# Performance work log

Measured on AMD Instinct MI355X. Metric: run time of the kernel, lower is better.

The kernel has to match this reference:

```python
import jax, jax.numpy as jnp
import numpy as np

B, S, D, H = 4, 2048, 1024, 16
HD = D // H  # 64


def setup_inputs() -> dict:
    key = jax.random.key(0)
    ks = jax.random.split(key, 16)
    inv = 1.0 / np.sqrt(D)
    inv_hd = 1.0 / np.sqrt(D)
    inp = {
        "query": jax.random.normal(ks[0], (B, S, D), jnp.float32),
        "key": jax.random.normal(ks[1], (B, S, D), jnp.float32),
        "value": jax.random.normal(ks[2], (B, S, D), jnp.float32),
        # causal mask: True entries are masked out (masked_fill semantics)
        "mask": jnp.triu(jnp.ones((S, S), jnp.bool_), k=1),
        # weights stored [in, out] (math identical to torch x @ W.T)
        "Wq": jax.random.normal(ks[3], (D, D), jnp.float32) * inv,
        "Wk": jax.random.normal(ks[4], (D, D), jnp.float32) * inv,
        "Wv": jax.random.normal(ks[5], (D, D), jnp.float32) * inv,
        "wq_h": jax.random.normal(ks[6], (D, HD), jnp.float32) * inv_hd,
        "bq_h": jax.random.normal(ks[7], (HD,), jnp.float32) * inv_hd,
        "wk_h": jax.random.normal(ks[8], (D, HD), jnp.float32) * inv_hd,
        "bk_h": jax.random.normal(ks[9], (HD,), jnp.float32) * inv_hd,
        "wv_h": jax.random.normal(ks[10], (D, HD), jnp.float32) * inv_hd,
        "bv_h": jax.random.normal(ks[11], (HD,), jnp.float32) * inv_hd,
        "Wo": jax.random.normal(ks[12], (D, D), jnp.float32) * inv,
    }
    return inp


def reference(query, key, value, mask, Wq, Wk, Wv, wq_h, bq_h, wk_h, bk_h, wv_h, bv_h, Wo):
    # full-width projections
    q = jnp.einsum('bsd,de->bse', query, Wq)
    k = jnp.einsum('bsd,de->bse', key, Wk)
    v = jnp.einsum('bsd,de->bse', value, Wv)
    # per-head projections: the torch loop reuses the SAME weights every
    # iteration, so all H head outputs are identical -> compute once.
    qh = jnp.einsum('bsd,dh->bsh', q, wq_h) + bq_h  # [B,S,HD]
    kh = jnp.einsum('bsd,dh->bsh', k, wk_h) + bk_h
    vh = jnp.einsum('bsd,dh->bsh', v, wv_h) + bv_h
    scores = jnp.einsum('bsh,bth->bst', qh, kh) / jnp.sqrt(jnp.float32(HD))
    scores = jnp.where(mask, jnp.float32(-1e9), scores)
    attn = jax.nn.softmax(scores, axis=-1)
    out_h = jnp.einsum('bst,bth->bsh', attn, vh)  # [B,S,HD]
    out = jnp.tile(out_h, (1, 1, H))  # cat of H identical heads -> [B,S,D]
    # final linear; dropout is identity at inference
    return jnp.einsum('bsd,de->bse', out, Wo)
```

## Files before the change

### kernel.cpp

```cpp
#include <hip/hip_runtime.h>
#include <math.h>

#define S_LEN 2048
#define BATCH 4
#define DMODEL 1024
#define HDIM 64
#define NROWS (BATCH * S_LEN)

typedef __attribute__((ext_vector_type(8))) short bf16x8;
typedef __attribute__((ext_vector_type(4))) float f32x4;

__device__ inline ushort f2bf(float f) {
    union { float f; uint u; } v{f};
    uint r = v.u + 0x7fffu + ((v.u >> 16) & 1u);
    return (ushort)(r >> 16);
}

__device__ inline bf16x8 cvt8(float4 a, float4 b) {
    bf16x8 r;
    r[0] = (short)f2bf(a.x); r[1] = (short)f2bf(a.y);
    r[2] = (short)f2bf(a.z); r[3] = (short)f2bf(a.w);
    r[4] = (short)f2bf(b.x); r[5] = (short)f2bf(b.y);
    r[6] = (short)f2bf(b.z); r[7] = (short)f2bf(b.w);
    return r;
}

__global__ __launch_bounds__(256) void transpose_wh(
    const float* __restrict__ B0, const float* __restrict__ B1, const float* __restrict__ B2,
    ushort* __restrict__ T0, ushort* __restrict__ T1, ushort* __restrict__ T2)
{
    const int z = blockIdx.y;
    const float* B = (z == 0) ? B0 : (z == 1) ? B1 : B2;
    ushort* T      = (z == 0) ? T0 : (z == 1) ? T1 : T2;
    const int kr0 = blockIdx.x * 64;
    __shared__ ushort Ts[64][72];
    const int t = threadIdx.x;

    #pragma unroll
    for (int q = 0; q < 4; ++q) {
        int u   = t * 4 + q;
        int row = u >> 4;
        int c4  = (u & 15) << 2;
        float4 v = *reinterpret_cast<const float4*>(
            B + (size_t)(kr0 + row) * 64 + c4);
        Ts[row][c4 + 0] = f2bf(v.x); Ts[row][c4 + 1] = f2bf(v.y);
        Ts[row][c4 + 2] = f2bf(v.z); Ts[row][c4 + 3] = f2bf(v.w);
    }
    __syncthreads();
    #pragma unroll
    for (int q = 0; q < 2; ++q) {
        int u  = t * 2 + q;
        int h  = u >> 3;
        int k8 = (u & 7) << 3;
        uint4 o;
        uint* ow = reinterpret_cast<uint*>(&o);
        #pragma unroll
        for (int i = 0; i < 4; ++i)
            ow[i] = (uint)Ts[k8 + 2 * i][h] | ((uint)Ts[k8 + 2 * i + 1][h] << 16);
        *reinterpret_cast<uint4*>(T + (size_t)h * 1024 + kr0 + k8) = o;
    }
}

__global__ __launch_bounds__(256) void prep_direct(
    const float* __restrict__ A0, const float* __restrict__ A1, const float* __restrict__ A2,
    const ushort* __restrict__ W0, const ushort* __restrict__ W1, const ushort* __restrict__ W2,
    ushort* __restrict__ T0, ushort* __restrict__ T1, ushort* __restrict__ T2)
{
    const int z = blockIdx.y;
    const float* A  = (z == 0) ? A0 : (z == 1) ? A1 : A2;
    const ushort* W = (z == 0) ? W0 : (z == 1) ? W1 : W2;
    ushort* T       = (z == 0) ? T0 : (z == 1) ? T1 : T2;

    __shared__ float Pr[4][16][64];

    const int t    = threadIdx.x;
    const int w    = t >> 6;
    const int lane = t & 63;
    const int lg   = lane >> 4;
    const int lc   = lane & 15;
    const int r0   = blockIdx.x * 16;

    const float*  Ap = A + (size_t)(r0 + lc) * 1024 + (w << 8) + (lg << 3);
    const ushort* Bp = W + (size_t)lc * 1024 + (w << 8) + (lg << 3);

    f32x4 acc[4] = {};
    float4 a0[2], a1[2];
    uint4  bl[2][4];

    #pragma unroll
    for (int d = 0; d < 2; ++d) {
        a0[d] = *reinterpret_cast<const float4*>(Ap + d * 32);
        a1[d] = *reinterpret_cast<const float4*>(Ap + d * 32 + 4);
        #pragma unroll
        for (int n = 0; n < 4; ++n)
            bl[d][n] = *reinterpret_cast<const uint4*>(Bp + n * 16384 + d * 32);
    }

    #pragma unroll
    for (int ks = 0; ks < 8; ++ks) {
        const int d = ks & 1;
        bf16x8 af = cvt8(a0[d], a1[d]);
        bf16x8 bfr[4];
        #pragma unroll
        for (int n = 0; n < 4; ++n)
            bfr[n] = __builtin_bit_cast(bf16x8, bl[d][n]);
        if (ks < 6) {
            a0[d] = *reinterpret_cast<const float4*>(Ap + (ks + 2) * 32);
            a1[d] = *reinterpret_cast<const float4*>(Ap + (ks + 2) * 32 + 4);
            #pragma unroll
            for (int n = 0; n < 4; ++n)
                bl[d][n] = *reinterpret_cast<const uint4*>(Bp + n * 16384 + (ks + 2) * 32);
        }
        #pragma unroll
        for (int n = 0; n < 4; ++n)
            acc[n] = __builtin_amdgcn_mfma_f32_16x16x32_bf16(af, bfr[n], acc[n], 0, 0, 0);
    }

    #pragma unroll
    for (int n = 0; n < 4; ++n)
        #pragma unroll
        for (int reg = 0; reg < 4; ++reg)
            Pr[w][4 * lg + reg][16 * n + lc] = acc[n][reg];
    __syncthreads();

    const int row = t >> 4;
    const int col = (t & 15) << 2;
    float s[4];
    #pragma unroll
    for (int i = 0; i < 4; ++i)
        s[i] = Pr[0][row][col + i] + Pr[1][row][col + i] +
               Pr[2][row][col + i] + Pr[3][row][col + i];
    #pragma unroll
    for (int i = 0; i < 4; ++i)
        T[(size_t)(col + i) * 1024 + r0 + row] = f2bf(s[i]);
}

__global__ __launch_bounds__(256) void proj_direct(
    const float* __restrict__ A0, const float* __restrict__ A1, const float* __restrict__ A2,
    const ushort* __restrict__ W0, const ushort* __restrict__ W1, const ushort* __restrict__ W2,
    const float* __restrict__ b0, const float* __restrict__ b1, const float* __restrict__ b2,
    ushort* __restrict__ O0, ushort* __restrict__ O1, ushort* __restrict__ O2)
{
    const int z = blockIdx.y;
    const float* A    = (z == 0) ? A0 : (z == 1) ? A1 : A2;
    const ushort* W   = (z == 0) ? W0 : (z == 1) ? W1 : W2;
    const float* bias = (z == 0) ? b0 : (z == 1) ? b1 : b2;
    ushort* O         = (z == 0) ? O0 : (z == 1) ? O1 : O2;

    __shared__ float Pr[4][16][64];

    const int t    = threadIdx.x;
    const int w    = t >> 6;
    const int lane = t & 63;
    const int lg   = lane >> 4;
    const int lc   = lane & 15;
    const int r0   = blockIdx.x * 16;

    const float*  Ap = A + (size_t)(r0 + lc) * 1024 + (w << 8) + (lg << 3);
    const ushort* Bp = W + (size_t)lc * 1024 + (w << 8) + (lg << 3);

    f32x4 acc[4] = {};
    float4 a0[2], a1[2];
    uint4  bl[2][4];

    #pragma unroll
    for (int d = 0; d < 2; ++d) {
        a0[d] = *reinterpret_cast<const float4*>(Ap + d * 32);
        a1[d] = *reinterpret_cast<const float4*>(Ap + d * 32 + 4);
        #pragma unroll
        for (int n = 0; n < 4; ++n)
            bl[d][n] = *reinterpret_cast<const uint4*>(Bp + n * 16384 + d * 32);
    }

    #pragma unroll
    for (int ks = 0; ks < 8; ++ks) {
        const int d = ks & 1;
        bf16x8 af = cvt8(a0[d], a1[d]);
        bf16x8 bfr[4];
        #pragma unroll
        for (int n = 0; n < 4; ++n)
            bfr[n] = __builtin_bit_cast(bf16x8, bl[d][n]);
        if (ks < 6) {
            a0[d] = *reinterpret_cast<const float4*>(Ap + (ks + 2) * 32);
            a1[d] = *reinterpret_cast<const float4*>(Ap + (ks + 2) * 32 + 4);
            #pragma unroll
            for (int n = 0; n < 4; ++n)
                bl[d][n] = *reinterpret_cast<const uint4*>(Bp + n * 16384 + (ks + 2) * 32);
        }
        #pragma unroll
        for (int n = 0; n < 4; ++n)
            acc[n] = __builtin_amdgcn_mfma_f32_16x16x32_bf16(af, bfr[n], acc[n], 0, 0, 0);
    }

    #pragma unroll
    for (int n = 0; n < 4; ++n)
        #pragma unroll
        for (int reg = 0; reg < 4; ++reg)
            Pr[w][4 * lg + reg][16 * n + lc] = acc[n][reg];
    __syncthreads();

    const int row = t >> 4;
    const int col = (t & 15) << 2;
    float4 bb = *reinterpret_cast<const float4*>(bias + col);
    float s0 = Pr[0][row][col + 0] + Pr[1][row][col + 0] + Pr[2][row][col + 0] + Pr[3][row][col + 0] + bb.x;
    float s1 = Pr[0][row][col + 1] + Pr[1][row][col + 1] + Pr[2][row][col + 1] + Pr[3][row][col + 1] + bb.y;
    float s2 = Pr[0][row][col + 2] + Pr[1][row][col + 2] + Pr[2][row][col + 2] + Pr[3][row][col + 2] + bb.z;
    float s3 = Pr[0][row][col + 3] + Pr[1][row][col + 3] + Pr[2][row][col + 3] + Pr[3][row][col + 3] + bb.w;
    ushort4 o;
    o.x = f2bf(s0); o.y = f2bf(s1); o.z = f2bf(s2); o.w = f2bf(s3);
    *reinterpret_cast<ushort4*>(O + (size_t)(r0 + row) * 64 + col) = o;
}

__global__ __launch_bounds__(256) void fold_wo(const float* __restrict__ Wo,
                                               ushort* __restrict__ WoT)
{
    int idx = blockIdx.x * 256 + threadIdx.x;
    int j = idx >> 10;
    int e = idx & 1023;
    float s = 0.f;
    #pragma unroll
    for (int h = 0; h < 16; ++h)
        s += Wo[(size_t)((h << 6) + j) * 1024 + e];
    WoT[(size_t)e * 64 + j] = f2bf(s);
}

__global__ __launch_bounds__(256) void transpose_v(const ushort* __restrict__ vh,
                                                   ushort* __restrict__ vhT)
{
    const int b  = blockIdx.y;
    const int r0 = blockIdx.x * 64;
    __shared__ ushort T[64][72];
    const int t = threadIdx.x;

    #pragma unroll
    for (int q = 0; q < 2; ++q) {
        int u  = t * 2 + q;
        int s  = u >> 3;
        int d8 = (u & 7) << 3;
        uint4 v = *reinterpret_cast<const uint4*>(
            vh + ((size_t)b * S_LEN + r0 + s) * 64 + d8);
        *reinterpret_cast<uint4*>(&T[s][d8]) = v;
    }
    __syncthreads();
    #pragma unroll
    for (int q = 0; q < 2; ++q) {
        int u  = t * 2 + q;
        int d  = u >> 3;
        int s8 = (u & 7) << 3;
        uint4 o;
        uint* ow = reinterpret_cast<uint*>(&o);
        #pragma unroll
        for (int i = 0; i < 4; ++i)
            ow[i] = (uint)T[s8 + 2 * i][d] | ((uint)T[s8 + 2 * i + 1][d] << 16);
        *reinterpret_cast<uint4*>(
            vhT + (size_t)b * 64 * S_LEN + (size_t)d * S_LEN + r0 + s8) = o;
    }
}

__global__ __launch_bounds__(256) void flash_mfma(
    const ushort* __restrict__ qh, const ushort* __restrict__ kh,
    const ushort* __restrict__ vhT,
    float* __restrict__ Opart, float* __restrict__ mpart, float* __restrict__ lpart)
{
    const int b = blockIdx.y;
    const int u = blockIdx.x;
    int gi = 0;
    #pragma unroll
    for (int gg = 0; gg < 7; ++gg)
        if (u >= 2 * (gg + 1) * (gg + 2)) gi = gg + 1;
    const int rem = u - 2 * gi * (gi + 1);
    const int dq  = rem / (gi + 1);
    const int c   = rem - dq * (gi + 1);
    const int qt  = 4 * gi + dq;
    const int r0  = qt * 64;
    const int kvbase = c << 8;
    const int slot = b * 144 + u;

    __shared__ ushort Qs[64][72];
    __shared__ ushort Ks[64][72];
    __shared__ ushort Vt[64][72];
    __shared__ ushort Pw[4][16][72];

    const int t    = threadIdx.x;
    const int w    = t >> 6;
    const int lane = t & 63;
    const int lg   = lane >> 4;
    const int lc   = lane & 15;

    const ushort* qb  = qh  + (size_t)b * S_LEN * 64;
    const ushort* kb  = kh  + (size_t)b * S_LEN * 64;
    const ushort* vtb = vhT + (size_t)b * 64 * S_LEN;

    #pragma unroll
    for (int q = 0; q < 2; ++q) {
        int uu  = t * 2 + q;
        int row = uu >> 3;
        int c8  = (uu & 7) << 3;
        *reinterpret_cast<uint4*>(&Qs[row][c8]) =
            *reinterpret_cast<const uint4*>(qb + (size_t)(r0 + row) * 64 + c8);
    }
    __syncthreads();
    bf16x8 qf0 = *reinterpret_cast<const bf16x8*>(&Qs[16 * w + lc][lg * 8]);
    bf16x8 qf1 = *reinterpret_cast<const bf16x8*>(&Qs[16 * w + lc][32 + lg * 8]);

    f32x4 od[4] = {};
    float m = -INFINITY, lsum = 0.f;
    const int qrow = r0 + 16 * w + lc;

    const int ntt = min(4, ((r0 + 63 - kvbase) >> 6) + 1);
    for (int tt = 0; tt < ntt; ++tt) {
        const int t0 = kvbase + (tt << 6);
        __syncthreads();
        #pragma unroll
        for (int q = 0; q < 2; ++q) {
            int uu  = t * 2 + q;
            int row = uu >> 3;
            int c8  = (uu & 7) << 3;
            *reinterpret_cast<uint4*>(&Ks[row][c8]) =
                *reinterpret_cast<const uint4*>(kb + (size_t)(t0 + row) * 64 + c8);
            *reinterpret_cast<uint4*>(&Vt[row][c8]) =
                *reinterpret_cast<const uint4*>(vtb + (size_t)row * S_LEN + t0 + c8);
        }
        __syncthreads();

        if (t0 <= r0 + 16 * w + 15) {
            f32x4 s[4] = {};
            #pragma unroll
            for (int a = 0; a < 4; ++a) {
                bf16x8 kf0 = *reinterpret_cast<const bf16x8*>(&Ks[16 * a + lc][lg * 8]);
                bf16x8 kf1 = *reinterpret_cast<const bf16x8*>(&Ks[16 * a + lc][32 + lg * 8]);
                s[a] = __builtin_amdgcn_mfma_f32_16x16x32_bf16(kf0, qf0, s[a], 0, 0, 0);
                s[a] = __builtin_amdgcn_mfma_f32_16x16x32_bf16(kf1, qf1, s[a], 0, 0, 0);
            }
            float rm = -1e30f;
            #pragma unroll
            for (int a = 0; a < 4; ++a)
                #pragma unroll
                for (int reg = 0; reg < 4; ++reg) {
                    int kv = t0 + 16 * a + 4 * lg + reg;
                    float v = s[a][reg] * 0.125f;
                    if (kv > qrow) v = -1e30f;
                    s[a][reg] = v;
                    rm = fmaxf(rm, v);
                }
            rm = fmaxf(rm, __shfl_xor(rm, 16));
            rm = fmaxf(rm, __shfl_xor(rm, 32));
            float mn = fmaxf(m, rm);
            float sc = __expf(m - mn);
            float rs = 0.f;
            #pragma unroll
            for (int a = 0; a < 4; ++a)
                #pragma unroll
                for (int reg = 0; reg < 4; ++reg) {
                    float p = __expf(s[a][reg] - mn);
                    s[a][reg] = p;
                    rs += p;
                }
            rs += __shfl_xor(rs, 16);
            rs += __shfl_xor(rs, 32);
            lsum = lsum * sc + rs;
            m = mn;
            #pragma unroll
            for (int di = 0; di < 4; ++di) od[di] *= sc;

            #pragma unroll
            for (int a = 0; a < 4; ++a)
                #pragma unroll
                for (int rp = 0; rp < 2; ++rp) {
                    uint pk = (uint)f2bf(s[a][2 * rp]) |
                              ((uint)f2bf(s[a][2 * rp + 1]) << 16);
                    *reinterpret_cast<uint*>(&Pw[w][lc][16 * a + 4 * lg + 2 * rp]) = pk;
                }
            bf16x8 pf0 = *reinterpret_cast<const bf16x8*>(&Pw[w][lc][lg * 8]);
            bf16x8 pf1 = *reinterpret_cast<const bf16x8*>(&Pw[w][lc][32 + lg * 8]);
            #pragma unroll
            for (int di = 0; di < 4; ++di) {
                bf16x8 vf0 = *reinterpret_cast<const bf16x8*>(&Vt[16 * di + lc][lg * 8]);
                bf16x8 vf1 = *reinterpret_cast<const bf16x8*>(&Vt[16 * di + lc][32 + lg * 8]);
                od[di] = __builtin_amdgcn_mfma_f32_16x16x32_bf16(vf0, pf0, od[di], 0, 0, 0);
                od[di] = __builtin_amdgcn_mfma_f32_16x16x32_bf16(vf1, pf1, od[di], 0, 0, 0);
            }
        }
    }

    #pragma unroll
    for (int di = 0; di < 4; ++di)
        #pragma unroll
        for (int reg = 0; reg < 4; ++reg)
            Opart[(size_t)slot * 4096 + (16 * di + 4 * lg + reg) * 64 + 16 * w + lc] =
                od[di][reg];
    if (lg == 0) {
        mpart[slot * 64 + 16 * w + lc] = m;
        lpart[slot * 64 + 16 * w + lc] = lsum;
    }
}

__global__ __launch_bounds__(256) void flash_combine(
    const float* __restrict__ Opart, const float* __restrict__ mpart,
    const float* __restrict__ lpart, ushort* __restrict__ oh)
{
    const int qt = blockIdx.x, b = blockIdx.y;
    const int gi = qt >> 2;
    const int nc = gi + 1;
    const int ubase = 2 * gi * (gi + 1) + (qt & 3) * (gi + 1);
    __shared__ float T[64][65];

    const int t  = threadIdx.x;
    const int q  = t & 63;
    const int d0 = (t >> 6) << 4;

    float mc[8];
    float M = -INFINITY;
    #pragma unroll
    for (int cc = 0; cc < 8; ++cc) {
        mc[cc] = (cc < nc) ? mpart[(b * 144 + ubase + cc) * 64 + q] : -INFINITY;
        M = fmaxf(M, mc[cc]);
    }
    float L = 0.f;
    float acc[16] = {};
    for (int cc = 0; cc < nc; ++cc) {
        const int slot = b * 144 + ubase + cc;
        float wgt = __expf(mc[cc] - M);
        L += lpart[slot * 64 + q] * wgt;
        const float* op = Opart + (size_t)slot * 4096 + q;
        #pragma unroll
        for (int i = 0; i < 16; ++i)
            acc[i] += wgt * op[(d0 + i) * 64];
    }
    float inv = 1.f / L;
    #pragma unroll
    for (int i = 0; i < 16; ++i) T[q][d0 + i] = acc[i] * inv;
    __syncthreads();

    const int q2 = t >> 2;
    const int ds = (t & 3) << 4;
    uint wbuf[8];
    #pragma unroll
    for (int i = 0; i < 8; ++i)
        wbuf[i] = (uint)f2bf(T[q2][ds + 2 * i]) |
                  ((uint)f2bf(T[q2][ds + 2 * i + 1]) << 16);
    ushort* dst = oh + ((size_t)b * S_LEN + qt * 64 + q2) * 64 + ds;
    uint4 o1, o2;
    o1.x = wbuf[0]; o1.y = wbuf[1]; o1.z = wbuf[2]; o1.w = wbuf[3];
    o2.x = wbuf[4]; o2.y = wbuf[5]; o2.z = wbuf[6]; o2.w = wbuf[7];
    *reinterpret_cast<uint4*>(dst)     = o1;
    *reinterpret_cast<uint4*>(dst + 8) = o2;
}

__global__ __launch_bounds__(256) void epilogue_mfma(
    const ushort* __restrict__ oh, const ushort* __restrict__ WoT,
    float* __restrict__ out)
{
    const int r0 = blockIdx.x * 64;
    const int c0 = blockIdx.y * 128;
    __shared__ ushort As[64][72];
    __shared__ ushort Bs[128][72];

    const int t    = threadIdx.x;
    const int w    = t >> 6;
    const int lane = t & 63;
    const int lg   = lane >> 4;
    const int lc   = lane & 15;

    #pragma unroll
    for (int q = 0; q < 2; ++q) {
        int u   = t * 2 + q;
        int row = u >> 3;
        int c8  = (u & 7) << 3;
        *reinterpret_cast<uint4*>(&As[row][c8]) =
            *reinterpret_cast<const uint4*>(oh + (size_t)(r0 + row) * 64 + c8);
    }
    #pragma unroll
    for (int q = 0; q < 4; ++q) {
        int u   = t * 4 + q;
        int row = u >> 3;
        int c8  = (u & 7) << 3;
        *reinterpret_cast<uint4*>(&Bs[row][c8]) =
            *reinterpret_cast<const uint4*>(WoT + (size_t)(c0 + row) * 64 + c8);
    }
    __syncthreads();

    bf16x8 af0 = *reinterpret_cast<const bf16x8*>(&As[16 * w + lc][lg * 8]);
    bf16x8 af1 = *reinterpret_cast<const bf16x8*>(&As[16 * w + lc][32 + lg * 8]);
    f32x4 acc[8] = {};
    #pragma unroll
    for (int n = 0; n < 8; ++n) {
        bf16x8 bf0 = *reinterpret_cast<const bf16x8*>(&Bs[16 * n + lc][lg * 8]);
        bf16x8 bf1 = *reinterpret_cast<const bf16x8*>(&Bs[16 * n + lc][32 + lg * 8]);
        acc[n] = __builtin_amdgcn_mfma_f32_16x16x32_bf16(af0, bf0, acc[n], 0, 0, 0);
        acc[n] = __builtin_amdgcn_mfma_f32_16x16x32_bf16(af1, bf1, acc[n], 0, 0, 0);
    }
    #pragma unroll
    for (int n = 0; n < 8; ++n)
        #pragma unroll
        for (int reg = 0; reg < 4; ++reg)
            out[(size_t)(r0 + 16 * w + 4 * lg + reg) * 1024 + c0 + 16 * n + lc] =
                acc[n][reg];
}

extern "C" void kernel_launch(void* const* d_in, const int* in_sizes, int n_in,
                              void* d_out, int out_size, void* d_ws, size_t ws_size,
                              hipStream_t stream)
{
    const float* query = (const float*)d_in[0];
    const float* key   = (const float*)d_in[1];
    const float* value = (const float*)d_in[2];
    const float* Wq   = (const float*)d_in[4];
    const float* Wk   = (const float*)d_in[5];
    const float* Wv   = (const float*)d_in[6];
    const float* wq_h = (const float*)d_in[7];
    const float* bq_h = (const float*)d_in[8];
    const float* wk_h = (const float*)d_in[9];
    const float* bk_h = (const float*)d_in[10];
    const float* wv_h = (const float*)d_in[11];
    const float* bv_h = (const float*)d_in[12];
    const float* Wo   = (const float*)d_in[13];
    float* out = (float*)d_out;

    ushort* W16  = (ushort*)d_ws;
    ushort* WT0  = W16;
    ushort* WT1  = W16 + 65536;
    ushort* WT2  = W16 + 131072;
    ushort* WoT  = W16 + 196608;
    ushort* qh   = W16 + 262144;
    ushort* kh   = qh + 524288;
    ushort* vh   = kh + 524288;
    ushort* vhT  = vh + 524288;
    ushort* oh   = vhT + 524288;
    ushort* whT0 = oh + 524288;
    ushort* whT1 = whT0 + 65536;
    ushort* whT2 = whT1 + 65536;

    float* Opart = out;
    float* mpart = out + 2359296;
    float* lpart = out + 2396160;

    transpose_wh<<<dim3(16, 3), 256, 0, stream>>>(
        wq_h, wk_h, wv_h, whT0, whT1, whT2);
    fold_wo<<<256, 256, 0, stream>>>(Wo, WoT);

    prep_direct<<<dim3(64, 3), 256, 0, stream>>>(
        Wq, Wk, Wv, whT0, whT1, whT2, WT0, WT1, WT2);

    proj_direct<<<dim3(512, 3), 256, 0, stream>>>(
        query, key, value, WT0, WT1, WT2, bq_h, bk_h, bv_h, qh, kh, vh);

    transpose_v<<<dim3(S_LEN / 64, BATCH), 256, 0, stream>>>(vh, vhT);

    flash_mfma<<<dim3(144, BATCH), 256, 0, stream>>>(
        qh, kh, vhT, Opart, mpart, lpart);
    flash_combine<<<dim3(S_LEN / 64, BATCH), 256, 0, stream>>>(
        Opart, mpart, lpart, oh);

    epilogue_mfma<<<dim3(NROWS / 64, DMODEL / 128), 256, 0, stream>>>(oh, WoT, out);
}
```

Baseline: 83.56 us.

## Stream projection activations through LDS with async global_load_lds and swizzle

The per-row projection kernel now loads its whole slice of folded weights into registers up front, then issues all activation loads as asynchronous global-to-LDS copies with an XOR swizzle. Each 64-column chunk is consumed once its copies land, using staged vmcnt waits, so MFMA work overlaps the remaining loads. The aim is deeper memory-level parallelism on the activation stream, which dominates this memory-bound kernel. In exchange it adds 64KB of LDS per block and a large register footprint for the weight fragments, both of which cut occupancy.

```diff
diff --git a/kernel.cpp b/kernel.cpp
--- a/kernel.cpp
+++ b/kernel.cpp
@@ -9,6 +9,9 @@
 
 typedef __attribute__((ext_vector_type(8))) short bf16x8;
 typedef __attribute__((ext_vector_type(4))) float f32x4;
+
+#define GLP(p) ((const __attribute__((address_space(1))) unsigned int*)(p))
+#define LDP(p) ((__attribute__((address_space(3))) unsigned int*)(p))
 
 __device__ inline ushort f2bf(float f) {
     union { float f; uint u; } v{f};
@@ -135,7 +138,7 @@
         T[(size_t)(col + i) * 1024 + r0 + row] = f2bf(s[i]);
 }
 
-__global__ __launch_bounds__(256) void proj_direct(
+__global__ __launch_bounds__(256) void proj_stream(
     const float* __restrict__ A0, const float* __restrict__ A1, const float* __restrict__ A2,
     const ushort* __restrict__ W0, const ushort* __restrict__ W1, const ushort* __restrict__ W2,
     const float* __restrict__ b0, const float* __restrict__ b1, const float* __restrict__ b2,
@@ -147,6 +150,7 @@
     const float* bias = (z == 0) ? b0 : (z == 1) ? b1 : b2;
     ushort* O         = (z == 0) ? O0 : (z == 1) ? O1 : O2;
 
+    __shared__ __align__(16) char StageRaw[65536];
     __shared__ float Pr[4][16][64];
 
     const int t    = threadIdx.x;
@@ -154,43 +158,66 @@
     const int lane = t & 63;
     const int lg   = lane >> 4;
     const int lc   = lane & 15;
+    const int rx   = lc & 7;
     const int r0   = blockIdx.x * 16;
 
-    const float*  Ap = A + (size_t)(r0 + lc) * 1024 + (w << 8) + (lg << 3);
-    const ushort* Bp = W + (size_t)lc * 1024 + (w << 8) + (lg << 3);
+    bf16x8 bB[4][4][2];
+    #pragma unroll
+    for (int c = 0; c < 4; ++c)
+        #pragma unroll
+        for (int n = 0; n < 4; ++n)
+            #pragma unroll
+            for (int h = 0; h < 2; ++h)
+                bB[c][n][h] = *reinterpret_cast<const bf16x8*>(
+                    W + (size_t)(16 * n + lc) * 1024 + (w << 8) + (c << 6) +
+                    h * 32 + lg * 8);
+    asm volatile("s_waitcnt vmcnt(0)" ::: "memory");
+    __builtin_amdgcn_sched_barrier(0);
+
+    #pragma unroll
+    for (int c = 0; c < 4; ++c)
+        #pragma unroll
+        for (int p = 0; p < 4; ++p) {
+            int u   = p * 64 + lane;
+            int row = u >> 4;
+            int pos = u & 15;
+            int g   = (pos & 8) | ((pos & 7) ^ (row & 7));
+            __builtin_amdgcn_global_load_lds(
+                GLP(A + (size_t)(r0 + row) * 1024 + (w << 8) + (c << 6) + g * 4),
+                LDP(StageRaw + (size_t)w * 16384 + c * 4096 + p * 1024),
+                16, 0, 0);
+        }
 
     f32x4 acc[4] = {};
-    float4 a0[2], a1[2];
-    uint4  bl[2][4];
-
-    #pragma unroll
-    for (int d = 0; d < 2; ++d) {
-        a0[d] = *reinterpret_cast<const float4*>(Ap + d * 32);
-        a1[d] = *reinterpret_cast<const float4*>(Ap + d * 32 + 4);
-        #pragma unroll
-        for (int n = 0; n < 4; ++n)
-            bl[d][n] = *reinterpret_cast<const uint4*>(Bp + n * 16384 + d * 32);
-    }
-
-    #pragma unroll
-    for (int ks = 0; ks < 8; ++ks) {
-        const int d = ks & 1;
-        bf16x8 af = cvt8(a0[d], a1[d]);
-        bf16x8 bfr[4];
-        #pragma unroll
-        for (int n = 0; n < 4; ++n)
-            bfr[n] = __builtin_bit_cast(bf16x8, bl[d][n]);
-        if (ks < 6) {
-            a0[d] = *reinterpret_cast<const float4*>(Ap + (ks + 2) * 32);
-            a1[d] = *reinterpret_cast<const float4*>(Ap + (ks + 2) * 32 + 4);
-            #pragma unroll
-            for (int n = 0; n < 4; ++n)
-                bl[d][n] = *reinterpret_cast<const uint4*>(Bp + n * 16384 + (ks + 2) * 32);
-        }
-        #pragma unroll
-        for (int n = 0; n < 4; ++n)
-            acc[n] = __builtin_amdgcn_mfma_f32_16x16x32_bf16(af, bfr[n], acc[n], 0, 0, 0);
-    }
+    const float4* lpw = reinterpret_cast<const float4*>(
+        StageRaw + (size_t)w * 16384);
+
+#define PROJ_CHUNK(c, VM)                                                     \
+    {                                                                         \
+        asm volatile("s_waitcnt vmcnt(" #VM ")" ::: "memory");                \
+        __builtin_amdgcn_sched_barrier(0);                                    \
+        const float4* lp = lpw + (c) * 256 + lc * 16;                         \
+        float4 f0 = lp[( (lg * 2 + 0) ^ rx)];                                 \
+        float4 f1 = lp[( (lg * 2 + 1) ^ rx)];                                 \
+        float4 f2 = lp[(8 | ((lg * 2 + 0) ^ rx))];                            \
+        float4 f3 = lp[(8 | ((lg * 2 + 1) ^ rx))];                            \
+        bf16x8 a0 = cvt8(f0, f1);                                             \
+        bf16x8 a1 = cvt8(f2, f3);                                             \
+        acc[0] = __builtin_amdgcn_mfma_f32_16x16x32_bf16(a0, bB[c][0][0], acc[0], 0, 0, 0); \
+        acc[0] = __builtin_amdgcn_mfma_f32_16x16x32_bf16(a1, bB[c][0][1], acc[0], 0, 0, 0); \
+        acc[1] = __builtin_amdgcn_mfma_f32_16x16x32_bf16(a0, bB[c][1][0], acc[1], 0, 0, 0); \
+        acc[1] = __builtin_amdgcn_mfma_f32_16x16x32_bf16(a1, bB[c][1][1], acc[1], 0, 0, 0); \
+        acc[2] = __builtin_amdgcn_mfma_f32_16x16x32_bf16(a0, bB[c][2][0], acc[2], 0, 0, 0); \
+        acc[2] = __builtin_amdgcn_mfma_f32_16x16x32_bf16(a1, bB[c][2][1], acc[2], 0, 0, 0); \
+        acc[3] = __builtin_amdgcn_mfma_f32_16x16x32_bf16(a0, bB[c][3][0], acc[3], 0, 0, 0); \
+        acc[3] = __builtin_amdgcn_mfma_f32_16x16x32_bf16(a1, bB[c][3][1], acc[3], 0, 0, 0); \
+    }
+
+    PROJ_CHUNK(0, 12)
+    PROJ_CHUNK(1, 8)
+    PROJ_CHUNK(2, 4)
+    PROJ_CHUNK(3, 0)
+#undef PROJ_CHUNK
 
     #pragma unroll
     for (int n = 0; n < 4; ++n)
@@ -542,7 +569,7 @@
     prep_direct<<<dim3(64, 3), 256, 0, stream>>>(
         Wq, Wk, Wv, whT0, whT1, whT2, WT0, WT1, WT2);
 
-    proj_direct<<<dim3(512, 3), 256, 0, stream>>>(
+    proj_stream<<<dim3(512, 3), 256, 0, stream>>>(
         query, key, value, WT0, WT1, WT2, bq_h, bk_h, bv_h, qh, kh, vh);
 
     transpose_v<<<dim3(S_LEN / 64, BATCH), 256, 0, stream>>>(vh, vhT);
```

Measured after the change: 83.16 us. No clear change (-0.5%).

## Rewrite projection kernel as single-wave blocks with swizzled LDS A staging

Applied to the files above, without the earlier changes.

The fused-weight projection kernel moves from four waves splitting K (with an LDS cross-wave reduction) to one 64-thread wave per 16-row block that walks the full K=1024. A tiles are loaded with coalesced float4 row reads, converted to bf16, and staged through a double-buffered XOR-swizzled LDS buffer to reach the MFMA operand layout, which removes the shared-memory partial-sum reduction and the block barrier. The tradeoff is fewer threads per block and a longer serial K loop per wave. Weight fragments are now read directly per chunk without prefetch, and no barrier protects the LDS reuse, which is only safe because the block is a single wave.

```diff
diff --git a/kernel.cpp b/kernel.cpp
--- a/kernel.cpp
+++ b/kernel.cpp
@@ -135,7 +135,7 @@
         T[(size_t)(col + i) * 1024 + r0 + row] = f2bf(s[i]);
 }
 
-__global__ __launch_bounds__(256) void proj_direct(
+__global__ __launch_bounds__(64) void proj_sw(
     const float* __restrict__ A0, const float* __restrict__ A1, const float* __restrict__ A2,
     const ushort* __restrict__ W0, const ushort* __restrict__ W1, const ushort* __restrict__ W2,
     const float* __restrict__ b0, const float* __restrict__ b1, const float* __restrict__ b2,
@@ -147,68 +147,75 @@
     const float* bias = (z == 0) ? b0 : (z == 1) ? b1 : b2;
     ushort* O         = (z == 0) ? O0 : (z == 1) ? O1 : O2;
 
-    __shared__ float Pr[4][16][64];
-
-    const int t    = threadIdx.x;
-    const int w    = t >> 6;
-    const int lane = t & 63;
-    const int lg   = lane >> 4;
-    const int lc   = lane & 15;
-    const int r0   = blockIdx.x * 16;
-
-    const float*  Ap = A + (size_t)(r0 + lc) * 1024 + (w << 8) + (lg << 3);
-    const ushort* Bp = W + (size_t)lc * 1024 + (w << 8) + (lg << 3);
+    __shared__ __align__(16) ushort Abuf[2][16][64];
+
+    const int l  = threadIdx.x;
+    const int lg = l >> 4;
+    const int lc = l & 15;
+    const int wu = lc >> 1;
+    const int wh = lc & 1;
+    const int r0 = blockIdx.x * 16;
 
     f32x4 acc[4] = {};
-    float4 a0[2], a1[2];
-    uint4  bl[2][4];
-
-    #pragma unroll
-    for (int d = 0; d < 2; ++d) {
-        a0[d] = *reinterpret_cast<const float4*>(Ap + d * 32);
-        a1[d] = *reinterpret_cast<const float4*>(Ap + d * 32 + 4);
-        #pragma unroll
-        for (int n = 0; n < 4; ++n)
-            bl[d][n] = *reinterpret_cast<const uint4*>(Bp + n * 16384 + d * 32);
-    }
-
-    #pragma unroll
-    for (int ks = 0; ks < 8; ++ks) {
-        const int d = ks & 1;
-        bf16x8 af = cvt8(a0[d], a1[d]);
-        bf16x8 bfr[4];
-        #pragma unroll
-        for (int n = 0; n < 4; ++n)
-            bfr[n] = __builtin_bit_cast(bf16x8, bl[d][n]);
-        if (ks < 6) {
-            a0[d] = *reinterpret_cast<const float4*>(Ap + (ks + 2) * 32);
-            a1[d] = *reinterpret_cast<const float4*>(Ap + (ks + 2) * 32 + 4);
-            #pragma unroll
-            for (int n = 0; n < 4; ++n)
-                bl[d][n] = *reinterpret_cast<const uint4*>(Bp + n * 16384 + (ks + 2) * 32);
-        }
-        #pragma unroll
-        for (int n = 0; n < 4; ++n)
-            acc[n] = __builtin_amdgcn_mfma_f32_16x16x32_bf16(af, bfr[n], acc[n], 0, 0, 0);
-    }
-
-    #pragma unroll
-    for (int n = 0; n < 4; ++n)
+
+#define LOADA(R, c)                                                           \
+    _Pragma("unroll")                                                         \
+    for (int j = 0; j < 4; ++j)                                               \
+        R[j] = *reinterpret_cast<const float4*>(                              \
+            A + (size_t)(r0 + 4 * j + lg) * 1024 + (c) * 64 + lc * 4);
+
+#define PROCESS(c, R, BUF)                                                    \
+    {                                                                         \
+        bf16x8 bfr[4][2];                                                     \
+        _Pragma("unroll")                                                     \
+        for (int a = 0; a < 4; ++a)                                           \
+            _Pragma("unroll")                                                 \
+            for (int s = 0; s < 2; ++s)                                       \
+                bfr[a][s] = *reinterpret_cast<const bf16x8*>(                 \
+                    W + (size_t)(16 * a + lc) * 1024 + (c) * 64 + s * 32 +    \
+                    lg * 8);                                                  \
+        _Pragma("unroll")                                                     \
+        for (int j = 0; j < 4; ++j) {                                         \
+            uint2 pk;                                                         \
+            pk.x = (uint)f2bf(R[j].x) | ((uint)f2bf(R[j].y) << 16);           \
+            pk.y = (uint)f2bf(R[j].z) | ((uint)f2bf(R[j].w) << 16);           \
+            int row = 4 * j + lg;                                             \
+            char* dst = (char*)Abuf + (BUF) * 2048 + row * 128 +              \
+                        ((wu ^ (row & 7)) << 4) + wh * 8;                     \
+            *reinterpret_cast<uint2*>(dst) = pk;                              \
+        }                                                                     \
+        _Pragma("unroll")                                                     \
+        for (int s = 0; s < 2; ++s) {                                         \
+            const char* src = (const char*)Abuf + (BUF) * 2048 + lc * 128 +   \
+                              (((s * 4 + lg) ^ (lc & 7)) << 4);               \
+            bf16x8 af = *reinterpret_cast<const bf16x8*>(src);                \
+            _Pragma("unroll")                                                 \
+            for (int a = 0; a < 4; ++a)                                       \
+                acc[a] = __builtin_amdgcn_mfma_f32_16x16x32_bf16(             \
+                    af, bfr[a][s], acc[a], 0, 0, 0);                          \
+        }                                                                     \
+    }
+
+    float4 ra[4], rb[4];
+    LOADA(ra, 0)
+    #pragma unroll
+    for (int cc = 0; cc < 8; ++cc) {
+        LOADA(rb, 2 * cc + 1)
+        PROCESS(2 * cc, ra, 0)
+        if (cc < 7) LOADA(ra, 2 * cc + 2)
+        PROCESS(2 * cc + 1, rb, 1)
+    }
+#undef LOADA
+#undef PROCESS
+
+    #pragma unroll
+    for (int a = 0; a < 4; ++a) {
+        float bv = bias[16 * a + lc];
         #pragma unroll
         for (int reg = 0; reg < 4; ++reg)
-            Pr[w][4 * lg + reg][16 * n + lc] = acc[n][reg];
-    __syncthreads();
-
-    const int row = t >> 4;
-    const int col = (t & 15) << 2;
-    float4 bb = *reinterpret_cast<const float4*>(bias + col);
-    float s0 = Pr[0][row][col + 0] + Pr[1][row][col + 0] + Pr[2][row][col + 0] + Pr[3][row][col + 0] + bb.x;
-    float s1 = Pr[0][row][col + 1] + Pr[1][row][col + 1] + Pr[2][row][col + 1] + Pr[3][row][col + 1] + bb.y;
-    float s2 = Pr[0][row][col + 2] + Pr[1][row][col + 2] + Pr[2][row][col + 2] + Pr[3][row][col + 2] + bb.z;
-    float s3 = Pr[0][row][col + 3] + Pr[1][row][col + 3] + Pr[2][row][col + 3] + Pr[3][row][col + 3] + bb.w;
-    ushort4 o;
-    o.x = f2bf(s0); o.y = f2bf(s1); o.z = f2bf(s2); o.w = f2bf(s3);
-    *reinterpret_cast<ushort4*>(O + (size_t)(r0 + row) * 64 + col) = o;
+            O[(size_t)(r0 + 4 * lg + reg) * 64 + 16 * a + lc] =
+                f2bf(acc[a][reg] + bv);
+    }
 }
 
 __global__ __launch_bounds__(256) void fold_wo(const float* __restrict__ Wo,
@@ -542,7 +549,7 @@
     prep_direct<<<dim3(64, 3), 256, 0, stream>>>(
         Wq, Wk, Wv, whT0, whT1, whT2, WT0, WT1, WT2);
 
-    proj_direct<<<dim3(512, 3), 256, 0, stream>>>(
+    proj_sw<<<dim3(512, 3), 64, 0, stream>>>(
         query, key, value, WT0, WT1, WT2, bq_h, bk_h, bv_h, qh, kh, vh);
 
     transpose_v<<<dim3(S_LEN / 64, BATCH), 256, 0, stream>>>(vh, vhT);
```

Result: slower. 85.81 us (+2.7%).

## Replace split-K register projection with LDS-tiled 64-row MFMA GEMM

Applied to the files above, without the earlier changes.

The fused per-head projection kernel no longer splits K across four waves with register prefetch and an LDS reduction. Each block now takes 64 rows, stages bf16-converted A tiles and weight tiles in shared memory per 64-wide K step, and each wave computes its own 16 rows over the full K. This lets the 64x1024 weight tile be shared by 64 rows instead of 16 and removes the cross-wave partial-sum reduction. In exchange it adds two barriers per K step, has no global-load prefetch, and launches a quarter as many blocks.

```diff
diff --git a/kernel.cpp b/kernel.cpp
--- a/kernel.cpp
+++ b/kernel.cpp
@@ -135,80 +135,73 @@
         T[(size_t)(col + i) * 1024 + r0 + row] = f2bf(s[i]);
 }
 
-__global__ __launch_bounds__(256) void proj_direct(
+__global__ __launch_bounds__(256) void proj_mfma(
     const float* __restrict__ A0, const float* __restrict__ A1, const float* __restrict__ A2,
     const ushort* __restrict__ W0, const ushort* __restrict__ W1, const ushort* __restrict__ W2,
     const float* __restrict__ b0, const float* __restrict__ b1, const float* __restrict__ b2,
     ushort* __restrict__ O0, ushort* __restrict__ O1, ushort* __restrict__ O2)
 {
     const int z = blockIdx.y;
-    const float* A    = (z == 0) ? A0 : (z == 1) ? A1 : A2;
-    const ushort* W   = (z == 0) ? W0 : (z == 1) ? W1 : W2;
+    const float* A  = (z == 0) ? A0 : (z == 1) ? A1 : A2;
+    const ushort* W = (z == 0) ? W0 : (z == 1) ? W1 : W2;
     const float* bias = (z == 0) ? b0 : (z == 1) ? b1 : b2;
-    ushort* O         = (z == 0) ? O0 : (z == 1) ? O1 : O2;
-
-    __shared__ float Pr[4][16][64];
+    ushort* O       = (z == 0) ? O0 : (z == 1) ? O1 : O2;
+
+    __shared__ ushort As[64][72];
+    __shared__ ushort Bs[64][72];
 
     const int t    = threadIdx.x;
     const int w    = t >> 6;
     const int lane = t & 63;
     const int lg   = lane >> 4;
     const int lc   = lane & 15;
-    const int r0   = blockIdx.x * 16;
-
-    const float*  Ap = A + (size_t)(r0 + lc) * 1024 + (w << 8) + (lg << 3);
-    const ushort* Bp = W + (size_t)lc * 1024 + (w << 8) + (lg << 3);
+    const int r0   = blockIdx.x * 64;
 
     f32x4 acc[4] = {};
-    float4 a0[2], a1[2];
-    uint4  bl[2][4];
-
-    #pragma unroll
-    for (int d = 0; d < 2; ++d) {
-        a0[d] = *reinterpret_cast<const float4*>(Ap + d * 32);
-        a1[d] = *reinterpret_cast<const float4*>(Ap + d * 32 + 4);
-        #pragma unroll
-        for (int n = 0; n < 4; ++n)
-            bl[d][n] = *reinterpret_cast<const uint4*>(Bp + n * 16384 + d * 32);
-    }
-
-    #pragma unroll
-    for (int ks = 0; ks < 8; ++ks) {
-        const int d = ks & 1;
-        bf16x8 af = cvt8(a0[d], a1[d]);
-        bf16x8 bfr[4];
-        #pragma unroll
-        for (int n = 0; n < 4; ++n)
-            bfr[n] = __builtin_bit_cast(bf16x8, bl[d][n]);
-        if (ks < 6) {
-            a0[d] = *reinterpret_cast<const float4*>(Ap + (ks + 2) * 32);
-            a1[d] = *reinterpret_cast<const float4*>(Ap + (ks + 2) * 32 + 4);
-            #pragma unroll
-            for (int n = 0; n < 4; ++n)
-                bl[d][n] = *reinterpret_cast<const uint4*>(Bp + n * 16384 + (ks + 2) * 32);
-        }
-        #pragma unroll
-        for (int n = 0; n < 4; ++n)
-            acc[n] = __builtin_amdgcn_mfma_f32_16x16x32_bf16(af, bfr[n], acc[n], 0, 0, 0);
-    }
-
-    #pragma unroll
-    for (int n = 0; n < 4; ++n)
-        #pragma unroll
-        for (int reg = 0; reg < 4; ++reg)
-            Pr[w][4 * lg + reg][16 * n + lc] = acc[n][reg];
-    __syncthreads();
-
-    const int row = t >> 4;
-    const int col = (t & 15) << 2;
-    float4 bb = *reinterpret_cast<const float4*>(bias + col);
-    float s0 = Pr[0][row][col + 0] + Pr[1][row][col + 0] + Pr[2][row][col + 0] + Pr[3][row][col + 0] + bb.x;
-    float s1 = Pr[0][row][col + 1] + Pr[1][row][col + 1] + Pr[2][row][col + 1] + Pr[3][row][col + 1] + bb.y;
-    float s2 = Pr[0][row][col + 2] + Pr[1][row][col + 2] + Pr[2][row][col + 2] + Pr[3][row][col + 2] + bb.z;
-    float s3 = Pr[0][row][col + 3] + Pr[1][row][col + 3] + Pr[2][row][col + 3] + Pr[3][row][col + 3] + bb.w;
-    ushort4 o;
-    o.x = f2bf(s0); o.y = f2bf(s1); o.z = f2bf(s2); o.w = f2bf(s3);
-    *reinterpret_cast<ushort4*>(O + (size_t)(r0 + row) * 64 + col) = o;
+
+    for (int k0 = 0; k0 < 1024; k0 += 64) {
+        __syncthreads();
+        #pragma unroll
+        for (int q = 0; q < 4; ++q) {
+            int u   = t * 4 + q;
+            int row = u >> 4;
+            int c4  = (u & 15) << 2;
+            float4 v = *reinterpret_cast<const float4*>(
+                A + (size_t)(r0 + row) * 1024 + k0 + c4);
+            ushort4 p;
+            p.x = f2bf(v.x); p.y = f2bf(v.y); p.z = f2bf(v.z); p.w = f2bf(v.w);
+            *reinterpret_cast<ushort4*>(&As[row][c4]) = p;
+        }
+        #pragma unroll
+        for (int q = 0; q < 2; ++q) {
+            int u   = t * 2 + q;
+            int row = u >> 3;
+            int c8  = (u & 7) << 3;
+            uint4 v = *reinterpret_cast<const uint4*>(W + (size_t)row * 1024 + k0 + c8);
+            *reinterpret_cast<uint4*>(&Bs[row][c8]) = v;
+        }
+        __syncthreads();
+
+        bf16x8 af0 = *reinterpret_cast<const bf16x8*>(&As[16 * w + lc][lg * 8]);
+        bf16x8 af1 = *reinterpret_cast<const bf16x8*>(&As[16 * w + lc][32 + lg * 8]);
+        #pragma unroll
+        for (int n = 0; n < 4; ++n) {
+            bf16x8 bf0 = *reinterpret_cast<const bf16x8*>(&Bs[16 * n + lc][lg * 8]);
+            bf16x8 bf1 = *reinterpret_cast<const bf16x8*>(&Bs[16 * n + lc][32 + lg * 8]);
+            acc[n] = __builtin_amdgcn_mfma_f32_16x16x32_bf16(af0, bf0, acc[n], 0, 0, 0);
+            acc[n] = __builtin_amdgcn_mfma_f32_16x16x32_bf16(af1, bf1, acc[n], 0, 0, 0);
+        }
+    }
+
+    #pragma unroll
+    for (int n = 0; n < 4; ++n) {
+        float bv = bias[16 * n + lc];
+        #pragma unroll
+        for (int reg = 0; reg < 4; ++reg) {
+            int row = r0 + 16 * w + 4 * lg + reg;
+            O[(size_t)row * 64 + 16 * n + lc] = f2bf(acc[n][reg] + bv);
+        }
+    }
 }
 
 __global__ __launch_bounds__(256) void fold_wo(const float* __restrict__ Wo,
@@ -542,7 +535,7 @@
     prep_direct<<<dim3(64, 3), 256, 0, stream>>>(
         Wq, Wk, Wv, whT0, whT1, whT2, WT0, WT1, WT2);
 
-    proj_direct<<<dim3(512, 3), 256, 0, stream>>>(
+    proj_mfma<<<dim3(NROWS / 64, 3), 256, 0, stream>>>(
         query, key, value, WT0, WT1, WT2, bq_h, bk_h, bv_h, qh, kh, vh);
 
     transpose_v<<<dim3(S_LEN / 64, BATCH), 256, 0, stream>>>(vh, vhT);
```

Result: faster. 75.81 us (-9.3%).
